# Optimization experiments

Measured on AMD Instinct MI355X. Metric: run time of the kernel, lower is better.

Reference implementation:

```python
import jax, jax.numpy as jnp
from jax import lax
import numpy as np

# --- constants matching harris_laplace_detector_batch defaults ---
NUM_OCTAVES = 6
INITIAL_SIGMA = 1.4
HARRIS_K = 0.04
THRESHOLD = 0.01

SOBEL_X = jnp.array([[-1., 0., 1.], [-2., 0., 2.], [-1., 0., 1.]], jnp.float32)
SOBEL_Y = SOBEL_X.T
# OpenCV Laplacian kernel for ksize=3
LAP3 = jnp.array([[2., 0., 2.], [0., -8., 0.], [2., 0., 2.]], jnp.float32)


def _conv2d(x, k):
    """Cross-correlate x [N,H,W] with kernel k [kh,kw], reflect-101 padding (cv2 default)."""
    kh, kw = k.shape
    pt, pb = kh // 2, kh - 1 - kh // 2
    pl, pr = kw // 2, kw - 1 - kw // 2
    xp = jnp.pad(x, ((0, 0), (pt, pb), (pl, pr)), mode='reflect')
    out = lax.conv_general_dilated(xp[:, None], k[None, None], (1, 1), 'VALID')
    return out[:, 0]


def _gaussian_blur(x, sigma):
    """Separable Gaussian blur, truncated at ~3 sigma (static kernel size per octave)."""
    r = max(1, int(3.0 * sigma + 0.5))
    t = jnp.arange(-r, r + 1, dtype=jnp.float32)
    g = jnp.exp(-0.5 * (t / sigma) ** 2)
    g = g / g.sum()
    x = _conv2d(x, g[None, :])  # blur rows
    x = _conv2d(x, g[:, None])  # blur cols
    return x


def setup_inputs() -> dict:
    key = jax.random.key(0)
    images = jax.random.uniform(key, (16, 3, 512, 512), dtype=jnp.float32)
    return {"images": images}


def reference(images) -> jnp.ndarray:
    B, C, H, W = images.shape
    x = images.reshape(B * C, H, W)  # treat each channel independently, as the torch loop does

    # cv2.normalize(..., 0, 255, NORM_MINMAX) per channel (continuous analogue of uint8 cast)
    mn = x.min(axis=(1, 2), keepdims=True)
    mx = x.max(axis=(1, 2), keepdims=True)
    gray = (x - mn) / (mx - mn + 1e-12) * 255.0

    # Harris response: Sobel gradients (ksize=3), 2x2 unnormalized box sum (blockSize=2)
    Ix = _conv2d(gray, SOBEL_X)
    Iy = _conv2d(gray, SOBEL_Y)
    box = jnp.ones((2, 2), jnp.float32)
    Sxx = _conv2d(Ix * Ix, box)
    Syy = _conv2d(Iy * Iy, box)
    Sxy = _conv2d(Ix * Iy, box)
    R = Sxx * Syy - Sxy * Sxy - HARRIS_K * (Sxx + Syy) ** 2

    # cv2.dilate with default 3x3 kernel = 3x3 max filter
    Rd = lax.reduce_window(R, -jnp.inf, lax.max, (1, 3, 3), (1, 1, 1), 'SAME')
    mask = (Rd > THRESHOLD * Rd.max(axis=(1, 2), keepdims=True)).astype(jnp.float32)

    # multi-octave |scaled Laplacian| blurred at each sigma, max-combined
    lap_base = _conv2d(gray, LAP3)
    combined = jnp.zeros_like(gray)
    for octave in range(NUM_OCTAVES):
        sigma = INITIAL_SIGMA * (2.0 ** octave)
        lap = jnp.abs(_gaussian_blur(lap_base * sigma, sigma))
        combined = jnp.maximum(combined, mask * lap)

    # max over channels (the torch loop keeps running np.maximum across channels)
    corners = combined.reshape(B, C, H, W).max(axis=1, keepdims=True)  # [B,1,H,W]
    return corners
```

## Files before the change

### kernel.cpp

```cpp
#include <hip/hip_runtime.h>

#define W 512
#define NPX (512*512)
#define NCH 48
#define NBATCH 16

__device__ __forceinline__ int refl(int i) {
    int a = i < 0 ? -i : i;
    int b = 1022 - a;
    return a < b ? a : b;
}
__device__ __forceinline__ unsigned encf(float f) {
    unsigned u = __float_as_uint(f);
    return (u & 0x80000000u) ? ~u : (u | 0x80000000u);
}
__device__ __forceinline__ float decf(unsigned e) {
    unsigned u = (e & 0x80000000u) ? (e & 0x7FFFFFFFu) : ~e;
    return __uint_as_float(u);
}
__device__ __forceinline__ unsigned long long enc64(double d) {
    unsigned long long u = (unsigned long long)__double_as_longlong(d);
    return (u & 0x8000000000000000ULL) ? ~u : (u | 0x8000000000000000ULL);
}
__device__ __forceinline__ double dec64(unsigned long long e) {
    unsigned long long u = (e & 0x8000000000000000ULL) ? (e & 0x7FFFFFFFFFFFFFFFULL) : ~e;
    return __longlong_as_double((long long)u);
}

__global__ void initK(unsigned* minenc, unsigned* maxenc, unsigned long long* rmaxenc,
                      unsigned* rowact, unsigned* colBits) {
    int t = threadIdx.x;
    if (t < NCH) { minenc[t] = 0xFFFFFFFFu; maxenc[t] = 0u; rmaxenc[t] = 0ULL; }
    for (int i = t; i < NCH*16; i += 1024) { rowact[i] = 0u; colBits[i] = 0u; }
}

__global__ void gaussK(float* gw) {
    int o = blockIdx.x;
    const int rr[6] = {4, 8, 17, 34, 67, 134};
    int r = rr[o];
    float sigma = 1.4f * (float)(1 << o);
    int t = threadIdx.x;
    int n = 2*r + 1;
    float wv = 0.f;
    if (t < n) { float ft = (float)(t - r) / sigma; wv = expf(-0.5f * ft * ft); }
    __shared__ float red[512];
    red[t] = wv; __syncthreads();
    for (int s = 256; s > 0; s >>= 1) { if (t < s) red[t] += red[t + s]; __syncthreads(); }
    float sum = red[0];
    float* g = gw + o*288;
    if (t < 288) g[t] = (t < n) ? wv / sum : 0.f;
}

__global__ void minmaxK(const float4* __restrict__ x4, unsigned* minenc, unsigned* maxenc) {
    int ch = blockIdx.y, chunk = blockIdx.x, t = threadIdx.x;
    size_t base = (size_t)ch*(NPX/4) + (size_t)chunk*8192;
    float mn = 3.4e38f, mx = -3.4e38f;
    for (int i = t; i < 8192; i += 256) {
        float4 v = x4[base + i];
        mn = fminf(mn, fminf(fminf(v.x, v.y), fminf(v.z, v.w)));
        mx = fmaxf(mx, fmaxf(fmaxf(v.x, v.y), fmaxf(v.z, v.w)));
    }
    for (int o = 32; o; o >>= 1) { mn = fminf(mn, __shfl_down(mn, o)); mx = fmaxf(mx, __shfl_down(mx, o)); }
    __shared__ float smn[4], smx[4];
    if ((t & 63) == 0) { smn[t >> 6] = mn; smx[t >> 6] = mx; }
    __syncthreads();
    if (t == 0) {
        for (int i = 1; i < 4; i++) { mn = fminf(mn, smn[i]); mx = fmaxf(mx, smx[i]); }
        atomicMin(&minenc[ch], encf(mn));
        atomicMax(&maxenc[ch], encf(mx));
    }
}

__global__ void scaleK(const unsigned* minenc, const unsigned* maxenc, double* gsd) {
    int t = threadIdx.x;
    if (t >= NCH) return;
    double mn = (double)decf(minenc[t]), mx = (double)decf(maxenc[t]);
    gsd[t] = 255.0 / (mx - mn + 1e-12);
}

__global__ __launch_bounds__(256) void lapRK(const float* __restrict__ x, const double* __restrict__ gsd,
                      float* __restrict__ lap, double* __restrict__ Rb,
                      unsigned long long* __restrict__ rmaxenc) {
    __shared__ float in[36*36];
    int ch = blockIdx.z;
    int px0 = blockIdx.x * 32, py0 = blockIdx.y * 32;
    const float* s = x + (size_t)ch*NPX;
    int t = threadIdx.x;
    for (int i = t; i < 36*36; i += 256) {
        int yy = i / 36, xx = i - yy*36;
        in[i] = s[(size_t)refl(py0 - 2 + yy)*W + refl(px0 - 2 + xx)];
    }
    __syncthreads();
    double sd = gsd[ch], s2 = sd*sd;
    int tx = t & 31, ty0 = (t >> 5) * 4;
    int gx = px0 + tx;
    int cb = gx ? tx : 1;
    double m = -1e308;
    #pragma unroll
    for (int q = 0; q < 4; q++) {
        int ly = ty0 + q;
        int gy = py0 + ly;
        int rb = gy ? ly : 1;
        double w[4][4];
        #pragma unroll
        for (int j = 0; j < 4; j++) {
            const float* rp = &in[(rb + j)*36 + cb];
            w[j][0] = (double)rp[0]; w[j][1] = (double)rp[1];
            w[j][2] = (double)rp[2]; w[j][3] = (double)rp[3];
        }
        double cs1[4], cs2[4], rs[4][2];
        #pragma unroll
        for (int c2 = 0; c2 < 4; c2++) {
            cs1[c2] = w[0][c2] + 2.0*w[1][c2] + w[2][c2];
            cs2[c2] = w[1][c2] + 2.0*w[2][c2] + w[3][c2];
        }
        #pragma unroll
        for (int j = 0; j < 4; j++) {
            rs[j][0] = w[j][0] + 2.0*w[j][1] + w[j][2];
            rs[j][1] = w[j][1] + 2.0*w[j][2] + w[j][3];
        }
        double Sxx = 0, Syy = 0, Sxy = 0;
        {
            double ix, iy;
            ix = cs1[2]-cs1[0]; iy = rs[2][0]-rs[0][0]; Sxx += ix*ix; Syy += iy*iy; Sxy += ix*iy;
            ix = cs1[3]-cs1[1]; iy = rs[2][1]-rs[0][1]; Sxx += ix*ix; Syy += iy*iy; Sxy += ix*iy;
            ix = cs2[2]-cs2[0]; iy = rs[3][0]-rs[1][0]; Sxx += ix*ix; Syy += iy*iy; Sxy += ix*iy;
            ix = cs2[3]-cs2[1]; iy = rs[3][1]-rs[1][1]; Sxx += ix*ix; Syy += iy*iy; Sxy += ix*iy;
        }
        Sxx *= s2; Syy *= s2; Sxy *= s2;
        double tr = Sxx + Syy;
        double R = Sxx*Syy - Sxy*Sxy - 0.04*tr*tr;
        Rb[(size_t)ch*NPX + (size_t)gy*W + gx] = R;
        const float* c = &in[(ly+2)*36 + (tx+2)];
        double l = 2.0*((double)c[-37] + (double)c[-35] + (double)c[35] + (double)c[37]) - 8.0*(double)c[0];
        lap[(size_t)ch*NPX + (size_t)gy*W + gx] = (float)(sd * l);
        m = fmax(m, R);
    }
    for (int o = 32; o; o >>= 1) m = fmax(m, __shfl_down(m, o));
    __shared__ double sred[4];
    if ((t & 63) == 0) sred[t >> 6] = m;
    __syncthreads();
    if (t == 0) {
        for (int i = 1; i < 4; i++) m = fmax(m, sred[i]);
        atomicMax(&rmaxenc[ch], enc64(m));
    }
}

__global__ __launch_bounds__(256) void maskTK(const double* __restrict__ Rb,
                                              const unsigned long long* __restrict__ rmaxenc,
                                              unsigned char* __restrict__ maskT,
                                              unsigned* __restrict__ rowact,
                                              unsigned* __restrict__ colBits) {
    __shared__ int bt[34*34];
    __shared__ unsigned char vt[32][33];
    __shared__ unsigned rw, cw;
    int ch = blockIdx.z;
    int px0 = blockIdx.x*32, py0 = blockIdx.y*32;
    double thr = 0.01 * dec64(rmaxenc[ch]);
    const double* R = Rb + (size_t)ch*NPX;
    int t = threadIdx.x;
    if (t == 0) { rw = 0u; cw = 0u; }
    for (int i = t; i < 34*34; i += 256) {
        int yy = i / 34, xx = i - yy*34;
        int gy = py0 - 1 + yy, gx = px0 - 1 + xx;
        int v = 0;
        if ((unsigned)gy < 512u && (unsigned)gx < 512u) v = (R[(size_t)gy*W + gx] > thr) ? 1 : 0;
        bt[i] = v;
    }
    __syncthreads();
    int tx = t & 31, ty0 = (t >> 5) * 4;
    int colv = 0;
    #pragma unroll
    for (int q = 0; q < 4; q++) {
        int ly = ty0 + q;
        int c = (ly+1)*34 + tx + 1;
        int v = bt[c-35] | bt[c-34] | bt[c-33] | bt[c-1] | bt[c] | bt[c+1] | bt[c+33] | bt[c+34] | bt[c+35];
        vt[tx][ly] = (unsigned char)v;
        colv |= v;
        unsigned long long bal = __ballot(v != 0);
        int lane = t & 63;
        if (lane == 0 && (unsigned)bal) atomicOr(&rw, 1u << (ty0 + q));
        if (lane == 32 && (unsigned)(bal >> 32)) atomicOr(&rw, 1u << (ty0 + q));
    }
    if (colv) atomicOr(&cw, 1u << tx);
    __syncthreads();
    int xl = t >> 3, seg = t & 7;
    uchar4 u4 = make_uchar4(vt[xl][seg*4+0], vt[xl][seg*4+1], vt[xl][seg*4+2], vt[xl][seg*4+3]);
    *(uchar4*)(maskT + (size_t)ch*NPX + (size_t)(px0 + xl)*W + py0 + seg*4) = u4;
    if (t == 0) {
        if (rw) atomicOr(&rowact[ch*16 + (py0 >> 5)], rw);
        if (cw) atomicOr(&colBits[ch*16 + blockIdx.x], cw);
    }
}

__global__ __launch_bounds__(512, 8) void rowblurK2(const float* __restrict__ src, float* __restrict__ Tt,
                                                    const float* __restrict__ gwo, int r, int nc8,
                                                    const unsigned* __restrict__ rowact) {
    int ch = blockIdx.y;
    int row0 = blockIdx.x * 8;
    int t = threadIdx.x;
    {
        int lo = row0 - r; if (lo < 0) lo = 0;
        int hi = row0 + 7 + r; if (hi > 511) hi = 511;
        int w0 = lo >> 5, w1 = hi >> 5;
        int lane = t & 63;
        unsigned any = 0;
        if (lane <= w1 - w0) {
            int wi = w0 + lane;
            unsigned word = rowact[ch*16 + wi];
            int b0 = wi*32;
            int lo2 = lo > b0 ? lo - b0 : 0;
            int hi2 = hi < b0 + 31 ? hi - b0 : 31;
            unsigned mlo = ~0u << lo2;
            unsigned mhi = (hi2 == 31) ? ~0u : ((1u << (hi2 + 1)) - 1u);
            any = word & mlo & mhi;
        }
        if (!__any((int)(any != 0))) return;
    }
    __shared__ float ES[8*784];
    __shared__ float wls[288];
    int lr = t >> 6, xi = t & 63;
    for (int i = t; i < 288; i += 512) wls[i] = gwo[i];
    const float* s = src + (size_t)ch*NPX + (size_t)(row0 + lr)*W;
    int n = W + 2*r;
    float* ESr = ES + lr*784;
    for (int j = xi; j < 784; j += 64)
        ESr[(j & 7)*98 + (j >> 3)] = (j < n) ? s[refl(j - r)] : 0.f;
    __syncthreads();
    float a[8];
    #pragma unroll
    for (int m = 0; m < 8; m++) a[m] = 0.f;
    for (int cc = 0; cc < nc8; ++cc) {
        float wv[8], f[15];
        #pragma unroll
        for (int i = 0; i < 8; i++) wv[i] = wls[8*cc + i];
        #pragma unroll
        for (int j = 0; j < 15; j++) f[j] = ESr[(j & 7)*98 + (xi + cc + (j >> 3))];
        #pragma unroll
        for (int m = 0; m < 8; m++) {
            #pragma unroll
            for (int i = 0; i < 8; i++) a[m] = fmaf(wv[i], f[m + i], a[m]);
        }
    }
    __syncthreads();
    #pragma unroll
    for (int m = 0; m < 8; m++) ES[(8*xi + m)*9 + lr] = a[m];
    __syncthreads();
    {
        const float* o = ES + t*9;
        float4* d = (float4*)(Tt + (size_t)ch*NPX + (size_t)t*W + row0);
        d[0] = make_float4(o[0], o[1], o[2], o[3]);
        d[1] = make_float4(o[4], o[5], o[6], o[7]);
    }
}

template<int WRITE0>
__global__ __launch_bounds__(512, 8) void colblurK2(const float* __restrict__ Tt,
                                                    const unsigned char* __restrict__ maskT,
                                                    float* __restrict__ outT,
                                                    const float* __restrict__ gwo,
                                                    int r, int nc8, float sigma,
                                                    const unsigned* __restrict__ colBits) {
    __shared__ float ES[8*784];
    __shared__ float wls[288];
    int b = blockIdx.y;
    int x0 = blockIdx.x * 8;
    int t = threadIdx.x;
    int lr = t >> 6, xi = t & 63;
    for (int i = t; i < 288; i += 512) wls[i] = gwo[i];
    float vm[8];
    #pragma unroll
    for (int m = 0; m < 8; m++) vm[m] = 0.f;
    int anyAct = 0;
    int n = W + 2*r;
    float* ESr = ES + lr*784;
    for (int c = 0; c < 3; ++c) {
        int ch = b*3 + c;
        unsigned cbits = (colBits[ch*16 + (x0 >> 5)] >> (x0 & 31)) & 0xFFu;
        if (!cbits) continue;
        anyAct = 1;
        __syncthreads();
        const float* s = Tt + (size_t)ch*NPX + (size_t)(x0 + lr)*W;
        for (int j = xi; j < 784; j += 64)
            ESr[(j & 7)*98 + (j >> 3)] = (j < n) ? s[refl(j - r)] : 0.f;
        __syncthreads();
        const uchar4* mp = (const uchar4*)(maskT + (size_t)ch*NPX + (size_t)(x0 + lr)*W + 8*xi);
        uchar4 m0 = mp[0], m1 = mp[1];
        unsigned mk = 0;
        mk |=  (m0.x?1u:0u)|(m0.y?2u:0u)|(m0.z?4u:0u)|(m0.w?8u:0u);
        mk |= ((m1.x?1u:0u)|(m1.y?2u:0u)|(m1.z?4u:0u)|(m1.w?8u:0u)) << 4;
        if (__any((int)(mk != 0))) {
            float a[8];
            #pragma unroll
            for (int m = 0; m < 8; m++) a[m] = 0.f;
            for (int cc = 0; cc < nc8; ++cc) {
                float wv[8], f[15];
                #pragma unroll
                for (int i = 0; i < 8; i++) wv[i] = wls[8*cc + i];
                #pragma unroll
                for (int j = 0; j < 15; j++) f[j] = ESr[(j & 7)*98 + (xi + cc + (j >> 3))];
                #pragma unroll
                for (int m = 0; m < 8; m++) {
                    #pragma unroll
                    for (int i = 0; i < 8; i++) a[m] = fmaf(wv[i], f[m + i], a[m]);
                }
            }
            #pragma unroll
            for (int m = 0; m < 8; m++)
                if (mk & (1u << m)) vm[m] = fmaxf(vm[m], sigma * fabsf(a[m]));
        }
    }
    if (!WRITE0 && !anyAct) return;
    float* ob = outT + (size_t)b*NPX + (size_t)(x0 + lr)*W + 8*xi;
    #pragma unroll
    for (int q = 0; q < 2; q++) {
        float4 vv = make_float4(vm[4*q], vm[4*q+1], vm[4*q+2], vm[4*q+3]);
        if (!WRITE0) {
            float4 cur = ((const float4*)ob)[q];
            vv.x = fmaxf(vv.x, cur.x); vv.y = fmaxf(vv.y, cur.y);
            vv.z = fmaxf(vv.z, cur.z); vv.w = fmaxf(vv.w, cur.w);
        }
        ((float4*)ob)[q] = vv;
    }
}

__global__ __launch_bounds__(256) void transposeK(const float* __restrict__ outT, float* __restrict__ out) {
    __shared__ float tl[32][33];
    int b = blockIdx.z;
    int x0 = blockIdx.x * 32, y0 = blockIdx.y * 32;
    int t = threadIdx.x;
    int col = t & 31, rr = t >> 5;
    const float* src = outT + (size_t)b*NPX;
    #pragma unroll
    for (int k = 0; k < 4; k++) {
        int xr = rr + 8*k;
        tl[xr][col] = src[(size_t)(x0 + xr)*W + y0 + col];
    }
    __syncthreads();
    float* d = out + (size_t)b*NPX;
    #pragma unroll
    for (int k = 0; k < 4; k++) {
        int yr = rr + 8*k;
        d[(size_t)(y0 + yr)*W + x0 + col] = tl[col][yr];
    }
}

extern "C" void kernel_launch(void* const* d_in, const int* in_sizes, int n_in,
                              void* d_out, int out_size, void* d_ws, size_t ws_size,
                              hipStream_t stream) {
    const float* x = (const float*)d_in[0];
    float* out = (float*)d_out;
    char* w = (char*)d_ws;
    unsigned* minenc           = (unsigned*)(w + 1024);
    unsigned* maxenc           = (unsigned*)(w + 1280);
    unsigned long long* rmaxenc= (unsigned long long*)(w + 1536);
    double*  gsd               = (double*)(w + 256);
    float*   gw                = (float*)(w + 2048);
    unsigned* rowact           = (unsigned*)(w + 9216);
    unsigned* colBits          = (unsigned*)(w + 12288);
    float*   lap               = (float*)(w + 16384);
    char*    rb                = w + 16384 + 50331648;
    double*  Rb                = (double*)rb;
    float*   Tt                = (float*)rb;
    float*   outT              = (float*)(rb + 50331648);
    unsigned char* maskT       = (unsigned char*)(w + 16384 + 50331648 + 100663296);

    initK<<<1, 1024, 0, stream>>>(minenc, maxenc, rmaxenc, rowact, colBits);
    gaussK<<<6, 512, 0, stream>>>(gw);
    minmaxK<<<dim3(8, 48), 256, 0, stream>>>((const float4*)x, minenc, maxenc);
    scaleK<<<1, 64, 0, stream>>>(minenc, maxenc, gsd);
    lapRK<<<dim3(16, 16, 48), 256, 0, stream>>>(x, gsd, lap, Rb, rmaxenc);
    maskTK<<<dim3(16, 16, 48), 256, 0, stream>>>(Rb, rmaxenc, maskT, rowact, colBits);

    const int rr[6] = {4, 8, 17, 34, 67, 134};
    for (int o = 0; o < 6; ++o) {
        int r = rr[o];
        int nc8 = (2*r + 1 + 7) / 8;
        float sigma = 1.4f * (float)(1 << o);
        rowblurK2<<<dim3(64, 48), 512, 0, stream>>>(lap, Tt, gw + o*288, r, nc8, rowact);
        if (o == 0)
            colblurK2<1><<<dim3(64, 16), 512, 0, stream>>>(Tt, maskT, outT, gw + o*288, r, nc8, sigma, colBits);
        else
            colblurK2<0><<<dim3(64, 16), 512, 0, stream>>>(Tt, maskT, outT, gw + o*288, r, nc8, sigma, colBits);
    }
    transposeK<<<dim3(16, 16, 16), 256, 0, stream>>>(outT, out);
}
```

Baseline: 812.9 us.

## Pre-pad transposed intermediate with reflected halo and vectorize blur staging loads

The row-blur pass now writes its transposed output into a 784-wide padded buffer that already holds the reflect-101 halo, so the column blur can stage rows with aligned float4 loads instead of per-element reflected gathers. Gaussian weights gain a front pad so the taps line up with 4-element alignment, and both blur kernels read the weights straight from global memory instead of copying them to shared memory. The row-blur activity check widens its window and drops one barrier. The cost is a larger intermediate buffer, extra scattered halo stores, and a few more taps per filter.

```diff
diff --git a/kernel.cpp b/kernel.cpp
--- a/kernel.cpp
+++ b/kernel.cpp
@@ -2,6 +2,7 @@
 
 #define W 512
 #define NPX (512*512)
+#define NPXT (512*784)
 #define NCH 48
 #define NBATCH 16
 
@@ -38,6 +39,7 @@
     int o = blockIdx.x;
     const int rr[6] = {4, 8, 17, 34, 67, 134};
     int r = rr[o];
+    int pre = (4 - (r & 3)) & 3;
     float sigma = 1.4f * (float)(1 << o);
     int t = threadIdx.x;
     int n = 2*r + 1;
@@ -47,8 +49,10 @@
     red[t] = wv; __syncthreads();
     for (int s = 256; s > 0; s >>= 1) { if (t < s) red[t] += red[t + s]; __syncthreads(); }
     float sum = red[0];
-    float* g = gw + o*288;
-    if (t < 288) g[t] = (t < n) ? wv / sum : 0.f;
+    float wv2 = 0.f;
+    int k = t - pre;
+    if (k >= 0 && k < n) { float ft = (float)(k - r) / sigma; wv2 = expf(-0.5f * ft * ft) / sum; }
+    if (t < 288) gw[o*288 + t] = wv2;
 }
 
 __global__ void minmaxK(const float4* __restrict__ x4, unsigned* minenc, unsigned* maxenc) {
@@ -194,14 +198,14 @@
 }
 
 __global__ __launch_bounds__(512, 8) void rowblurK2(const float* __restrict__ src, float* __restrict__ Tt,
-                                                    const float* __restrict__ gwo, int r, int nc8,
+                                                    const float* __restrict__ gwo, int r, int pre, int nc8,
                                                     const unsigned* __restrict__ rowact) {
     int ch = blockIdx.y;
     int row0 = blockIdx.x * 8;
     int t = threadIdx.x;
     {
-        int lo = row0 - r; if (lo < 0) lo = 0;
-        int hi = row0 + 7 + r; if (hi > 511) hi = 511;
+        int lo = row0 - r - 8; if (lo < 0) lo = 0;
+        int hi = row0 + 15 + r; if (hi > 511) hi = 511;
         int w0 = lo >> 5, w1 = hi >> 5;
         int lane = t & 63;
         unsigned any = 0;
@@ -218,22 +222,30 @@
         if (!__any((int)(any != 0))) return;
     }
     __shared__ float ES[8*784];
-    __shared__ float wls[288];
     int lr = t >> 6, xi = t & 63;
-    for (int i = t; i < 288; i += 512) wls[i] = gwo[i];
     const float* s = src + (size_t)ch*NPX + (size_t)(row0 + lr)*W;
-    int n = W + 2*r;
+    int rp = r + pre;
+    int nstage = 512 + 8*nc8;
     float* ESr = ES + lr*784;
-    for (int j = xi; j < 784; j += 64)
-        ESr[(j & 7)*98 + (j >> 3)] = (j < n) ? s[refl(j - r)] : 0.f;
-    __syncthreads();
+    for (int q = xi; q < 128; q += 64) {
+        float4 v = *(const float4*)(s + 4*q);
+        int e0 = rp + 4*q;
+        ESr[((e0+0)&7)*98 + ((e0+0)>>3)] = v.x;
+        ESr[((e0+1)&7)*98 + ((e0+1)>>3)] = v.y;
+        ESr[((e0+2)&7)*98 + ((e0+2)>>3)] = v.z;
+        ESr[((e0+3)&7)*98 + ((e0+3)>>3)] = v.w;
+    }
+    for (int e = xi; e < rp; e += 64)
+        ESr[(e&7)*98 + (e>>3)] = s[refl(e - rp)];
+    for (int e = rp + 512 + xi; e < nstage; e += 64)
+        ESr[(e&7)*98 + (e>>3)] = s[refl(e - rp)];
     float a[8];
     #pragma unroll
     for (int m = 0; m < 8; m++) a[m] = 0.f;
     for (int cc = 0; cc < nc8; ++cc) {
         float wv[8], f[15];
         #pragma unroll
-        for (int i = 0; i < 8; i++) wv[i] = wls[8*cc + i];
+        for (int i = 0; i < 8; i++) wv[i] = gwo[8*cc + i];
         #pragma unroll
         for (int j = 0; j < 15; j++) f[j] = ESr[(j & 7)*98 + (xi + cc + (j >> 3))];
         #pragma unroll
@@ -248,9 +260,18 @@
     __syncthreads();
     {
         const float* o = ES + t*9;
-        float4* d = (float4*)(Tt + (size_t)ch*NPX + (size_t)t*W + row0);
+        float* trow = Tt + (size_t)ch*NPXT + (size_t)t*784;
+        float4* d = (float4*)(trow + 136 + row0);
         d[0] = make_float4(o[0], o[1], o[2], o[3]);
         d[1] = make_float4(o[4], o[5], o[6], o[7]);
+        if (row0 <= 136 || row0 + 7 >= 375) {
+            #pragma unroll
+            for (int m = 0; m < 8; m++) {
+                int y = row0 + m;
+                if (y >= 1 && y <= 136)    trow[136 - y]  = o[m];
+                if (y >= 375 && y <= 510)  trow[1158 - y] = o[m];
+            }
+        }
     }
 }
 
@@ -259,31 +280,34 @@
                                                     const unsigned char* __restrict__ maskT,
                                                     float* __restrict__ outT,
                                                     const float* __restrict__ gwo,
-                                                    int r, int nc8, float sigma,
+                                                    int r, int pre, int nc8, float sigma,
                                                     const unsigned* __restrict__ colBits) {
     __shared__ float ES[8*784];
-    __shared__ float wls[288];
     int b = blockIdx.y;
     int x0 = blockIdx.x * 8;
     int t = threadIdx.x;
     int lr = t >> 6, xi = t & 63;
-    for (int i = t; i < 288; i += 512) wls[i] = gwo[i];
     float vm[8];
     #pragma unroll
     for (int m = 0; m < 8; m++) vm[m] = 0.f;
     int anyAct = 0;
-    int n = W + 2*r;
+    int base = 136 - r - pre;
+    int n4 = (512 + 8*nc8) >> 2;
     float* ESr = ES + lr*784;
     for (int c = 0; c < 3; ++c) {
         int ch = b*3 + c;
         unsigned cbits = (colBits[ch*16 + (x0 >> 5)] >> (x0 & 31)) & 0xFFu;
         if (!cbits) continue;
         anyAct = 1;
-        __syncthreads();
-        const float* s = Tt + (size_t)ch*NPX + (size_t)(x0 + lr)*W;
-        for (int j = xi; j < 784; j += 64)
-            ESr[(j & 7)*98 + (j >> 3)] = (j < n) ? s[refl(j - r)] : 0.f;
-        __syncthreads();
+        const float* s = Tt + (size_t)ch*NPXT + (size_t)(x0 + lr)*784 + base;
+        for (int q = xi; q < n4; q += 64) {
+            float4 v = *(const float4*)(s + 4*q);
+            int e0 = 4*q;
+            ESr[((e0+0)&7)*98 + ((e0+0)>>3)] = v.x;
+            ESr[((e0+1)&7)*98 + ((e0+1)>>3)] = v.y;
+            ESr[((e0+2)&7)*98 + ((e0+2)>>3)] = v.z;
+            ESr[((e0+3)&7)*98 + ((e0+3)>>3)] = v.w;
+        }
         const uchar4* mp = (const uchar4*)(maskT + (size_t)ch*NPX + (size_t)(x0 + lr)*W + 8*xi);
         uchar4 m0 = mp[0], m1 = mp[1];
         unsigned mk = 0;
@@ -296,7 +320,7 @@
             for (int cc = 0; cc < nc8; ++cc) {
                 float wv[8], f[15];
                 #pragma unroll
-                for (int i = 0; i < 8; i++) wv[i] = wls[8*cc + i];
+                for (int i = 0; i < 8; i++) wv[i] = gwo[8*cc + i];
                 #pragma unroll
                 for (int j = 0; j < 15; j++) f[j] = ESr[(j & 7)*98 + (xi + cc + (j >> 3))];
                 #pragma unroll
@@ -362,7 +386,7 @@
     char*    rb                = w + 16384 + 50331648;
     double*  Rb                = (double*)rb;
     float*   Tt                = (float*)rb;
-    float*   outT              = (float*)(rb + 50331648);
+    float*   outT              = (float*)(rb + 77070336);
     unsigned char* maskT       = (unsigned char*)(w + 16384 + 50331648 + 100663296);
 
     initK<<<1, 1024, 0, stream>>>(minenc, maxenc, rmaxenc, rowact, colBits);
@@ -375,13 +399,14 @@
     const int rr[6] = {4, 8, 17, 34, 67, 134};
     for (int o = 0; o < 6; ++o) {
         int r = rr[o];
-        int nc8 = (2*r + 1 + 7) / 8;
+        int pre = (4 - (r & 3)) & 3;
+        int nc8 = (pre + 2*r + 1 + 7) / 8;
         float sigma = 1.4f * (float)(1 << o);
-        rowblurK2<<<dim3(64, 48), 512, 0, stream>>>(lap, Tt, gw + o*288, r, nc8, rowact);
+        rowblurK2<<<dim3(64, 48), 512, 0, stream>>>(lap, Tt, gw + o*288, r, pre, nc8, rowact);
         if (o == 0)
-            colblurK2<1><<<dim3(64, 16), 512, 0, stream>>>(Tt, maskT, outT, gw + o*288, r, nc8, sigma, colBits);
+            colblurK2<1><<<dim3(64, 16), 512, 0, stream>>>(Tt, maskT, outT, gw + o*288, r, pre, nc8, sigma, colBits);
         else
-            colblurK2<0><<<dim3(64, 16), 512, 0, stream>>>(Tt, maskT, outT, gw + o*288, r, nc8, sigma, colBits);
+            colblurK2<0><<<dim3(64, 16), 512, 0, stream>>>(Tt, maskT, outT, gw + o*288, r, pre, nc8, sigma, colBits);
     }
     transposeK<<<dim3(16, 16, 16), 256, 0, stream>>>(outT, out);
 }
```

New measurement: 893.8 us. 1.1x slower.
